# Kernel tuning notes

Hardware: AMD Instinct MI355X
Metric: run time of the kernel (lower is better)

Reference implementation:

```python
import jax, jax.numpy as jnp
import numpy as np

N, L, D = 2, 2048, 96
H, DK, DV = 4, 16, 16
OUT = 96
SPATIAL = H * (3 + 1 + 3)  # points + distance + direction per head
INF = 100000.0
EPS_DIR = 1e-10
EPS_LN = 1e-5


def setup_inputs() -> dict:
    key = jax.random.key(0)
    ks = jax.random.split(key, 10)
    return {
        "x": jax.random.normal(ks[0], (N, L, D), jnp.float32),
        "pos_CA": jax.random.normal(ks[1], (N, L, 3), jnp.float32),
        "pos_CB": jax.random.normal(ks[2], (N, L, 3), jnp.float32),
        "frame": jax.random.normal(ks[3], (N, L, 3, 3), jnp.float32),
        "mask": jnp.ones((N, L), dtype=bool),
        "Wq": jax.random.normal(ks[4], (D, H * DK), jnp.float32) * 0.1,
        "Wk": jax.random.normal(ks[5], (D, H * DK), jnp.float32) * 0.1,
        "Wv": jax.random.normal(ks[6], (D, H * DV), jnp.float32) * 0.1,
        "Wo": jax.random.normal(ks[7], (H * DV + SPATIAL, OUT), jnp.float32) * 0.1,
        "bo": jnp.zeros((OUT,), jnp.float32),
        "gamma": jnp.ones((OUT,), jnp.float32),
        "beta": jnp.zeros((OUT,), jnp.float32),
    }


def reference(x, pos_CA, pos_CB, frame, mask, Wq, Wk, Wv, Wo, bo, gamma, beta):
    n, l, _ = x.shape
    q = (x @ Wq).reshape(n, l, H, DK)
    k = (x @ Wk).reshape(n, l, H, DK)
    v = (x @ Wv).reshape(n, l, H, DV)

    # logits (N, L_q, L_k, H)
    logits = jnp.einsum('blhd,bkhd->blkh', q, k)
    mask_row = mask[:, :, None, None]           # (N, L, 1, 1)
    mask_pair = mask_row & mask[:, None, :, None]
    logits = jnp.where(mask_pair, logits, logits - INF)
    alpha = jax.nn.softmax(logits, axis=2)
    alpha = jnp.where(mask_row, alpha, 0.0)

    feat_node = jnp.einsum('blkh,bkhd->blhd', alpha, v).reshape(n, l, H * DV)

    # rel_pos[b,l,k] = CB[k] - CA[l]
    rel_pos = pos_CB[:, None, :, :] - pos_CA[:, :, None, :]
    atom_pos_bias = jnp.einsum('blkh,blkd->blhd', alpha, rel_pos)  # (N,L,H,3)
    feat_distance = jnp.linalg.norm(atom_pos_bias, axis=-1, keepdims=True)
    feat_points = jnp.einsum('blij,blhj->blhi', frame, atom_pos_bias)
    feat_direction = feat_points / (jnp.linalg.norm(feat_points, axis=-1, keepdims=True) + EPS_DIR)

    feat_spatial = jnp.concatenate([
        feat_points.reshape(n, l, H * 3),
        feat_distance.reshape(n, l, H),
        feat_direction.reshape(n, l, H * 3),
    ], axis=-1)

    feat_all = jnp.concatenate([feat_node, feat_spatial], axis=-1) @ Wo + bo
    feat_all = jnp.where(mask[:, :, None], feat_all, 0.0)

    # output_dim == input_dim -> residual + LayerNorm
    h = x + feat_all
    mu = jnp.mean(h, axis=-1, keepdims=True)
    var = jnp.var(h, axis=-1, keepdims=True)
    return (h - mu) / jnp.sqrt(var + EPS_LN) * gamma + beta
```

## Files before the change

kernel.cpp:

```cpp
#include <hip/hip_runtime.h>
#include <hip/hip_fp16.h>

typedef _Float16 f16;
typedef _Float16 v4h __attribute__((ext_vector_type(4)));
typedef short    v4s __attribute__((ext_vector_type(4)));
typedef short    v8s __attribute__((ext_vector_type(8)));
typedef float    v4f __attribute__((ext_vector_type(4)));

#define NB   2
#define LSEQ 2048
#define DIM  96
#define NH   4
#define ROWS 4096
#define NT16 128
#define NT32 64
#define OUTD 96
#define SHIFT 12.0f

#if __has_builtin(__builtin_amdgcn_mfma_f32_16x16x16f16)
#define MFMA16_F16(A, B, C) __builtin_amdgcn_mfma_f32_16x16x16f16((A), (B), (C), 0, 0, 0)
#else
static __device__ __forceinline__ v4f mfma16_f16_asm(v4h a, v4h b, v4f c) {
    asm volatile("v_mfma_f32_16x16x16_f16 %0, %1, %2, %0"
                 : "+v"(c) : "v"(a), "v"(b));
    return c;
}
#define MFMA16_F16(A, B, C) mfma16_f16_asm((A), (B), (C))
#endif
#define MFMA_BF16(A, B, C) __builtin_amdgcn_mfma_f32_16x16x32_bf16((A), (B), (C), 0, 0, 0)

static __device__ __forceinline__ short f2bf(float f) {
    unsigned u = __builtin_bit_cast(unsigned, f);
    u += 0x7FFF + ((u >> 16) & 1);
    return (short)(u >> 16);
}

__global__ __launch_bounds__(256) void proj_kernel(
    const float* __restrict__ x,
    const float* __restrict__ posCB,
    const float* __restrict__ Wq,
    const float* __restrict__ Wk,
    const float* __restrict__ Wv,
    f16*   __restrict__ qf,
    f16*   __restrict__ kf,
    short* __restrict__ vf,
    short* __restrict__ pf)
{
    const int w    = threadIdx.x >> 6;
    const int lane = threadIdx.x & 63;
    const int rowbase = blockIdx.x * 4;

    __shared__ float xs[4][DIM];
    __shared__ float part[4][4][64][3];

    xs[w][lane] = x[(size_t)(rowbase + w) * DIM + lane];
    if (lane < DIM - 64) xs[w][64 + lane] = x[(size_t)(rowbase + w) * DIM + 64 + lane];
    __syncthreads();

    float qa[4] = {0.f, 0.f, 0.f, 0.f};
    float ka[4] = {0.f, 0.f, 0.f, 0.f};
    float va[4] = {0.f, 0.f, 0.f, 0.f};
    const int d0 = w * 24;
    #pragma unroll 6
    for (int t = 0; t < 24; ++t) {
        const int dd = d0 + t;
        const float wqv = Wq[dd * 64 + lane];
        const float wkv = Wk[dd * 64 + lane];
        const float wvv = Wv[dd * 64 + lane];
        #pragma unroll
        for (int r = 0; r < 4; ++r) {
            const float xv = xs[r][dd];
            qa[r] = fmaf(xv, wqv, qa[r]);
            ka[r] = fmaf(xv, wkv, ka[r]);
            va[r] = fmaf(xv, wvv, va[r]);
        }
    }
    #pragma unroll
    for (int r = 0; r < 4; ++r) {
        part[w][r][lane][0] = qa[r];
        part[w][r][lane][1] = ka[r];
        part[w][r][lane][2] = va[r];
    }
    __syncthreads();

    float q = 0.f, k = 0.f, v = 0.f;
    #pragma unroll
    for (int w2 = 0; w2 < 4; ++w2) {
        q += part[w2][w][lane][0];
        k += part[w2][w][lane][1];
        v += part[w2][w][lane][2];
    }
    const int row = rowbase + w;
    const int b   = row >> 11;
    const int seq = row & (LSEQ - 1);
    const int h   = lane >> 4, d = lane & 15;
    const int bh  = b * NH + h;

    const int t16 = seq >> 4, m = seq & 15;
    const int idx16 = (m + 16 * (d >> 2)) * 4 + (d & 3);
    qf[((size_t)(bh * NT16 + t16)) * 256 + idx16] = (f16)q;
    kf[((size_t)(bh * NT16 + t16)) * 256 + idx16] = (f16)k;

    const int t32 = seq >> 5, kl = seq & 31;
    const int quadS = (kl & 15) >> 2;
    const int jS    = (kl < 16) ? (kl & 3) : 4 + (kl & 3);
    vf[((size_t)(bh * NT32 + t32)) * 512 + (d + 16 * quadS) * 8 + jS] = f2bf(v);

    if (blockIdx.x < NB * NT32) {
        const int b2 = blockIdx.x >> 6, t2 = blockIdx.x & 63;
        const int tid = threadIdx.x;
        const int lf = tid & 63, jh = tid >> 6;
        const int n = lf & 15, qS = lf >> 4;
        #pragma unroll
        for (int u = 0; u < 2; ++u) {
            const int jSp = jh * 2 + u;
            const int key = t2 * 32 + (jSp < 4 ? qS * 4 + jSp : 16 + qS * 4 + (jSp & 3));
            float val = 0.f;
            if (n < 3)       val = posCB[((size_t)(b2 * LSEQ + key)) * 3 + n];
            else if (n == 3) val = 1.f;
            pf[((size_t)(b2 * NT32 + t2)) * 512 + lf * 8 + jSp] = f2bf(val);
        }
    }
}

__global__ __launch_bounds__(1024, 1) void attn_epi_kernel(
    const f16*   __restrict__ qf,
    const f16*   __restrict__ kf,
    const short* __restrict__ vf,
    const short* __restrict__ pf,
    const float* __restrict__ x,
    const float* __restrict__ posCA,
    const float* __restrict__ frame,
    const float* __restrict__ Wo,
    const float* __restrict__ bo,
    const float* __restrict__ gamma,
    const float* __restrict__ beta,
    float*       __restrict__ out)
{
    const int w     = threadIdx.x >> 6;
    const int lane  = threadIdx.x & 63;
    const int head  = w & 3, kq = w >> 2;
    const int b     = blockIdx.x >> 7;
    const int qt    = blockIdx.x & 127;
    const int bh    = b * NH + head;
    const int quad  = lane >> 4, c16 = lane & 15;

    __shared__ float comb[16][64][12];
    __shared__ float feat[16][100];
    __shared__ float aps[16][NH][3];

    const v4h aq = *(const v4h*)(qf + ((size_t)(bh * NT16 + qt)) * 256 + lane * 4);
    const f16*   kb = kf + (size_t)bh * NT16 * 256;
    const short* vb = vf + (size_t)bh * NT32 * 512;
    const short* pb = pf + (size_t)b  * NT32 * 512;

    v4f O  = {0.f, 0.f, 0.f, 0.f};
    v4f Wa = {0.f, 0.f, 0.f, 0.f};
    const v4f zero = {0.f, 0.f, 0.f, 0.f};
    float psum = 0.f;

    #pragma unroll 2
    for (int i = 0; i < 16; ++i) {
        const int t32 = kq * 16 + i;
        const v4h bk0 = *(const v4h*)(kb + (size_t)(2 * t32    ) * 256 + lane * 4);
        const v4h bk1 = *(const v4h*)(kb + (size_t)(2 * t32 + 1) * 256 + lane * 4);
        const v8s bv  = *(const v8s*)(vb + (size_t)t32 * 512 + lane * 8);
        const v8s bp  = *(const v8s*)(pb + (size_t)t32 * 512 + lane * 8);

        const v4f S0 = MFMA16_F16(bk0, aq, zero);
        const v4f S1 = MFMA16_F16(bk1, aq, zero);

        v8s ap;
        #pragma unroll
        for (int r = 0; r < 4; ++r) {
            const float e0 = __expf(S0[r] - SHIFT);
            const float e1 = __expf(S1[r] - SHIFT);
            ap[r]     = f2bf(e0);
            ap[4 + r] = f2bf(e1);
            psum += e0 + e1;
        }
        O  = MFMA_BF16(ap, bv, O);
        Wa = MFMA_BF16(ap, bp, Wa);
    }

    {
        float* cb = &comb[w][lane][0];
        *(v4f*)cb       = O;
        *(v4f*)(cb + 4) = Wa;
        cb[8] = psum;
    }
    __syncthreads();

    const int rowg0 = b * LSEQ + qt * 16;

    if (w < 4) {
        #pragma unroll
        for (int k2 = 1; k2 < 4; ++k2) {
            const float* cb = &comb[k2 * 4 + w][lane][0];
            O    += *(const v4f*)cb;
            Wa   += *(const v4f*)(cb + 4);
            psum += cb[8];
        }
        psum += __shfl_xor(psum, 16);
        psum += __shfl_xor(psum, 32);
        const float inv = 1.f / psum;
        #pragma unroll
        for (int r = 0; r < 4; ++r) {
            const float ir = __shfl(inv, quad * 4 + r);
            feat[quad * 4 + r][w * 16 + c16] = O[r] * ir;
            if (c16 < 3)
                aps[quad * 4 + r][w][c16] = Wa[r] * ir;
        }
    }
    __syncthreads();

    if (lane < 4) {
        const int hh = lane;
        const int grow = rowg0 + w;
        float apb[3];
        #pragma unroll
        for (int j = 0; j < 3; ++j)
            apb[j] = aps[w][hh][j] - posCA[(size_t)grow * 3 + j];
        const float dist = sqrtf(apb[0]*apb[0] + apb[1]*apb[1] + apb[2]*apb[2]);
        float fp[3];
        #pragma unroll
        for (int i = 0; i < 3; ++i) {
            float a = 0.f;
            #pragma unroll
            for (int j = 0; j < 3; ++j)
                a = fmaf(frame[(size_t)grow * 9 + i * 3 + j], apb[j], a);
            fp[i] = a;
        }
        const float fpn  = sqrtf(fp[0]*fp[0] + fp[1]*fp[1] + fp[2]*fp[2]);
        const float rinv = 1.f / (fpn + 1e-10f);
        #pragma unroll
        for (int i = 0; i < 3; ++i) {
            feat[w][64 + hh * 3 + i] = fp[i];
            feat[w][80 + hh * 3 + i] = fp[i] * rinv;
        }
        feat[w][76 + hh] = dist;
    }
    __syncthreads();

    {
        const int grow = rowg0 + w;

        float acc0 = bo[lane];
        #pragma unroll 8
        for (int r2 = 0; r2 < 92; ++r2)
            acc0 = fmaf(feat[w][r2], Wo[r2 * OUTD + lane], acc0);
        const float hv0 = acc0 + x[(size_t)grow * DIM + lane];

        float hv1 = 0.f;
        if (lane < 32) {
            float acc1 = bo[64 + lane];
            #pragma unroll 8
            for (int r2 = 0; r2 < 92; ++r2)
                acc1 = fmaf(feat[w][r2], Wo[r2 * OUTD + 64 + lane], acc1);
            hv1 = acc1 + x[(size_t)grow * DIM + 64 + lane];
        }

        float ls = hv0 + hv1;
        float lq = fmaf(hv0, hv0, hv1 * hv1);
        #pragma unroll
        for (int off = 32; off > 0; off >>= 1) {
            ls += __shfl_xor(ls, off);
            lq += __shfl_xor(lq, off);
        }
        const float mu  = ls * (1.f / OUTD);
        const float var = lq * (1.f / OUTD) - mu * mu;
        const float rs  = rsqrtf(var + 1e-5f);

        out[(size_t)grow * OUTD + lane] = (hv0 - mu) * rs * gamma[lane] + beta[lane];
        if (lane < 32)
            out[(size_t)grow * OUTD + 64 + lane] =
                (hv1 - mu) * rs * gamma[64 + lane] + beta[64 + lane];
    }
}

extern "C" void kernel_launch(void* const* d_in, const int* in_sizes, int n_in,
                              void* d_out, int out_size, void* d_ws, size_t ws_size,
                              hipStream_t stream)
{
    const float* x     = (const float*)d_in[0];
    const float* posCA = (const float*)d_in[1];
    const float* posCB = (const float*)d_in[2];
    const float* frame = (const float*)d_in[3];
    const float* Wq    = (const float*)d_in[5];
    const float* Wk    = (const float*)d_in[6];
    const float* Wv    = (const float*)d_in[7];
    const float* Wo    = (const float*)d_in[8];
    const float* bo    = (const float*)d_in[9];
    const float* gamma = (const float*)d_in[10];
    const float* beta  = (const float*)d_in[11];

    f16*   qf = (f16*)d_ws;
    f16*   kf = qf + (size_t)8 * NT16 * 256;
    short* vf = (short*)(kf + (size_t)8 * NT16 * 256);
    short* pf = vf + (size_t)8 * NT32 * 512;

    proj_kernel<<<ROWS / 4, 256, 0, stream>>>(x, posCB, Wq, Wk, Wv, qf, kf, vf, pf);
    attn_epi_kernel<<<NB * NT16, 1024, 0, stream>>>(qf, kf, vf, pf,
                                                    x, posCA, frame,
                                                    Wo, bo, gamma, beta,
                                                    (float*)d_out);
}
```

Before: 105.3 us.

## Use MFMA for QKV projection, pack K tiles pairwise, prefetch attention loads

The QKV projection now runs on f16 MFMA, with 16 rows per block and weights staged into LDS fragments. It replaces the scalar FMA loop and its cross-wave LDS reduction, and launches 256 blocks instead of 1024. K is stored in a packed 32-key layout so one 8-wide load feeds both score MFMAs. The attention loop software-prefetches the next tile's K/V/P and uses exp2 with a folded log2e and shift. Every block re-converts the full weight matrices into LDS, and rounding x and W to f16 slightly changes precision.

```diff
diff --git a/kernel.cpp b/kernel.cpp
--- a/kernel.cpp
+++ b/kernel.cpp
@@ -3,6 +3,7 @@
 
 typedef _Float16 f16;
 typedef _Float16 v4h __attribute__((ext_vector_type(4)));
+typedef _Float16 v8h __attribute__((ext_vector_type(8)));
 typedef short    v4s __attribute__((ext_vector_type(4)));
 typedef short    v8s __attribute__((ext_vector_type(8)));
 typedef float    v4f __attribute__((ext_vector_type(4)));
@@ -16,6 +17,8 @@
 #define NT32 64
 #define OUTD 96
 #define SHIFT 12.0f
+#define LOG2E   1.4426950408889634f
+#define NSH2    (-17.312340490667562f)
 
 #if __has_builtin(__builtin_amdgcn_mfma_f32_16x16x16f16)
 #define MFMA16_F16(A, B, C) __builtin_amdgcn_mfma_f32_16x16x16f16((A), (B), (C), 0, 0, 0)
@@ -27,7 +30,14 @@
 }
 #define MFMA16_F16(A, B, C) mfma16_f16_asm((A), (B), (C))
 #endif
-#define MFMA_BF16(A, B, C) __builtin_amdgcn_mfma_f32_16x16x32_bf16((A), (B), (C), 0, 0, 0)
+#define MFMA32_F16(A, B, C) __builtin_amdgcn_mfma_f32_16x16x32_f16((A), (B), (C), 0, 0, 0)
+#define MFMA_BF16(A, B, C)  __builtin_amdgcn_mfma_f32_16x16x32_bf16((A), (B), (C), 0, 0, 0)
+
+#if __has_builtin(__builtin_amdgcn_exp2f)
+#define EXP2F(x) __builtin_amdgcn_exp2f(x)
+#else
+#define EXP2F(x) exp2f(x)
+#endif
 
 static __device__ __forceinline__ short f2bf(float f) {
     unsigned u = __builtin_bit_cast(unsigned, f);
@@ -42,78 +52,87 @@
     const float* __restrict__ Wk,
     const float* __restrict__ Wv,
     f16*   __restrict__ qf,
-    f16*   __restrict__ kf,
+    f16*   __restrict__ kf2,
     short* __restrict__ vf,
     short* __restrict__ pf)
 {
-    const int w    = threadIdx.x >> 6;
-    const int lane = threadIdx.x & 63;
-    const int rowbase = blockIdx.x * 4;
-
-    __shared__ float xs[4][DIM];
-    __shared__ float part[4][4][64][3];
-
-    xs[w][lane] = x[(size_t)(rowbase + w) * DIM + lane];
-    if (lane < DIM - 64) xs[w][64 + lane] = x[(size_t)(rowbase + w) * DIM + 64 + lane];
+    const int tid  = threadIdx.x;
+    const int wv   = tid >> 6;
+    const int lane = tid & 63;
+    const int quad = lane >> 4, c16 = lane & 15;
+    const int bid  = blockIdx.x;
+    const int b    = bid >> 7, t16 = bid & 127;
+    const int row0 = bid * 16;
+
+    __shared__ v8h wfragv[12 * 3 * 65];
+    f16* wf = (f16*)wfragv;
+
+    v8h xb[3];
+    #pragma unroll
+    for (int kt = 0; kt < 3; ++kt) {
+        const float* xp = x + (size_t)(row0 + c16) * DIM + kt * 32 + quad * 8;
+        const v4f x0 = *(const v4f*)xp;
+        const v4f x1 = *(const v4f*)(xp + 4);
+        v8h h;
+        #pragma unroll
+        for (int j = 0; j < 4; ++j) { h[j] = (f16)x0[j]; h[4 + j] = (f16)x1[j]; }
+        xb[kt] = h;
+    }
+
+    {
+        const float* Ws[3] = {Wq, Wk, Wv};
+        #pragma unroll
+        for (int widx = 0; widx < 3; ++widx) {
+            const float* W = Ws[widx];
+            #pragma unroll
+            for (int it = 0; it < 24; ++it) {
+                const int flat = it * 256 + tid;
+                const int dd = flat >> 6, n = flat & 63;
+                const int frag = (widx * 4 + (n >> 4)) * 3 + (dd >> 5);
+                wf[frag * 520 + (((dd >> 3) & 3) * 16 + (n & 15)) * 8 + (dd & 7)]
+                    = (f16)W[flat];
+            }
+        }
+    }
     __syncthreads();
 
-    float qa[4] = {0.f, 0.f, 0.f, 0.f};
-    float ka[4] = {0.f, 0.f, 0.f, 0.f};
-    float va[4] = {0.f, 0.f, 0.f, 0.f};
-    const int d0 = w * 24;
-    #pragma unroll 6
-    for (int t = 0; t < 24; ++t) {
-        const int dd = d0 + t;
-        const float wqv = Wq[dd * 64 + lane];
-        const float wkv = Wk[dd * 64 + lane];
-        const float wvv = Wv[dd * 64 + lane];
-        #pragma unroll
-        for (int r = 0; r < 4; ++r) {
-            const float xv = xs[r][dd];
-            qa[r] = fmaf(xv, wqv, qa[r]);
-            ka[r] = fmaf(xv, wkv, ka[r]);
-            va[r] = fmaf(xv, wvv, va[r]);
-        }
-    }
     #pragma unroll
-    for (int r = 0; r < 4; ++r) {
-        part[w][r][lane][0] = qa[r];
-        part[w][r][lane][1] = ka[r];
-        part[w][r][lane][2] = va[r];
-    }
-    __syncthreads();
-
-    float q = 0.f, k = 0.f, v = 0.f;
-    #pragma unroll
-    for (int w2 = 0; w2 < 4; ++w2) {
-        q += part[w2][w][lane][0];
-        k += part[w2][w][lane][1];
-        v += part[w2][w][lane][2];
-    }
-    const int row = rowbase + w;
-    const int b   = row >> 11;
-    const int seq = row & (LSEQ - 1);
-    const int h   = lane >> 4, d = lane & 15;
-    const int bh  = b * NH + h;
-
-    const int t16 = seq >> 4, m = seq & 15;
-    const int idx16 = (m + 16 * (d >> 2)) * 4 + (d & 3);
-    qf[((size_t)(bh * NT16 + t16)) * 256 + idx16] = (f16)q;
-    kf[((size_t)(bh * NT16 + t16)) * 256 + idx16] = (f16)k;
-
-    const int t32 = seq >> 5, kl = seq & 31;
-    const int quadS = (kl & 15) >> 2;
-    const int jS    = (kl < 16) ? (kl & 3) : 4 + (kl & 3);
-    vf[((size_t)(bh * NT32 + t32)) * 512 + (d + 16 * quadS) * 8 + jS] = f2bf(v);
-
-    if (blockIdx.x < NB * NT32) {
-        const int b2 = blockIdx.x >> 6, t2 = blockIdx.x & 63;
-        const int tid = threadIdx.x;
+    for (int u = 0; u < 3; ++u) {
+        const int dt = wv * 3 + u;
+        v4f acc = {0.f, 0.f, 0.f, 0.f};
+        #pragma unroll
+        for (int kt = 0; kt < 3; ++kt)
+            acc = MFMA32_F16(wfragv[(dt * 3 + kt) * 65 + lane], xb[kt], acc);
+
+        const int widx = dt >> 2, sub = dt & 3;
+        const int bh = b * NH + sub;
+        if (widx == 0) {
+            v4h o;
+            #pragma unroll
+            for (int r = 0; r < 4; ++r) o[r] = (f16)acc[r];
+            *(v4h*)(qf + ((size_t)(bh * NT16 + t16)) * 256 + (c16 + 16 * quad) * 4) = o;
+        } else if (widx == 1) {
+            v4h o;
+            #pragma unroll
+            for (int r = 0; r < 4; ++r) o[r] = (f16)acc[r];
+            *(v4h*)(kf2 + ((size_t)(bh * NT32 + (t16 >> 1))) * 512
+                        + lane * 8 + (t16 & 1) * 4) = o;
+        } else {
+            short* dst = vf + ((size_t)(bh * NT32 + (t16 >> 1))) * 512
+                            + (t16 & 1) * 4 + (c16 & 3);
+            #pragma unroll
+            for (int r = 0; r < 4; ++r)
+                dst[(quad * 4 + r + 16 * (c16 >> 2)) * 8] = f2bf(acc[r]);
+        }
+    }
+
+    if (bid < NB * NT32) {
+        const int b2 = bid >> 6, t2 = bid & 63;
         const int lf = tid & 63, jh = tid >> 6;
         const int n = lf & 15, qS = lf >> 4;
         #pragma unroll
-        for (int u = 0; u < 2; ++u) {
-            const int jSp = jh * 2 + u;
+        for (int u2 = 0; u2 < 2; ++u2) {
+            const int jSp = jh * 2 + u2;
             const int key = t2 * 32 + (jSp < 4 ? qS * 4 + jSp : 16 + qS * 4 + (jSp & 3));
             float val = 0.f;
             if (n < 3)       val = posCB[((size_t)(b2 * LSEQ + key)) * 3 + n];
@@ -125,7 +144,7 @@
 
 __global__ __launch_bounds__(1024, 1) void attn_epi_kernel(
     const f16*   __restrict__ qf,
-    const f16*   __restrict__ kf,
+    const f16*   __restrict__ kf2,
     const short* __restrict__ vf,
     const short* __restrict__ pf,
     const float* __restrict__ x,
@@ -150,38 +169,49 @@
     __shared__ float aps[16][NH][3];
 
     const v4h aq = *(const v4h*)(qf + ((size_t)(bh * NT16 + qt)) * 256 + lane * 4);
-    const f16*   kb = kf + (size_t)bh * NT16 * 256;
-    const short* vb = vf + (size_t)bh * NT32 * 512;
-    const short* pb = pf + (size_t)b  * NT32 * 512;
+    const f16*   kb = kf2 + (size_t)bh * NT32 * 512;
+    const short* vb = vf  + (size_t)bh * NT32 * 512;
+    const short* pb = pf  + (size_t)b  * NT32 * 512;
 
     v4f O  = {0.f, 0.f, 0.f, 0.f};
     v4f Wa = {0.f, 0.f, 0.f, 0.f};
     const v4f zero = {0.f, 0.f, 0.f, 0.f};
     float psum = 0.f;
 
-    #pragma unroll 2
-    for (int i = 0; i < 16; ++i) {
-        const int t32 = kq * 16 + i;
-        const v4h bk0 = *(const v4h*)(kb + (size_t)(2 * t32    ) * 256 + lane * 4);
-        const v4h bk1 = *(const v4h*)(kb + (size_t)(2 * t32 + 1) * 256 + lane * 4);
-        const v8s bv  = *(const v8s*)(vb + (size_t)t32 * 512 + lane * 8);
-        const v8s bp  = *(const v8s*)(pb + (size_t)t32 * 512 + lane * 8);
-
-        const v4f S0 = MFMA16_F16(bk0, aq, zero);
-        const v4f S1 = MFMA16_F16(bk1, aq, zero);
-
-        v8s ap;
-        #pragma unroll
-        for (int r = 0; r < 4; ++r) {
-            const float e0 = __expf(S0[r] - SHIFT);
-            const float e1 = __expf(S1[r] - SHIFT);
-            ap[r]     = f2bf(e0);
-            ap[4 + r] = f2bf(e1);
-            psum += e0 + e1;
-        }
-        O  = MFMA_BF16(ap, bv, O);
-        Wa = MFMA_BF16(ap, bp, Wa);
-    }
+    const int t0 = kq * 16;
+    v8h bk = *(const v8h*)(kb + (size_t)t0 * 512 + lane * 8);
+    v8s bv = *(const v8s*)(vb + (size_t)t0 * 512 + lane * 8);
+    v8s bp = *(const v8s*)(pb + (size_t)t0 * 512 + lane * 8);
+
+#define ATTN_STEP(BK, BV, BP) do {                                          \
+        const v4h bk0 = __builtin_shufflevector((BK), (BK), 0, 1, 2, 3);    \
+        const v4h bk1 = __builtin_shufflevector((BK), (BK), 4, 5, 6, 7);    \
+        const v4f S0 = MFMA16_F16(bk0, aq, zero);                           \
+        const v4f S1 = MFMA16_F16(bk1, aq, zero);                           \
+        v8s ap;                                                             \
+        _Pragma("unroll")                                                   \
+        for (int r = 0; r < 4; ++r) {                                       \
+            const float e0 = EXP2F(fmaf(S0[r], LOG2E, NSH2));               \
+            const float e1 = EXP2F(fmaf(S1[r], LOG2E, NSH2));               \
+            ap[r]     = f2bf(e0);                                           \
+            ap[4 + r] = f2bf(e1);                                           \
+            psum += e0 + e1;                                                \
+        }                                                                   \
+        O  = MFMA_BF16(ap, (BV), O);                                        \
+        Wa = MFMA_BF16(ap, (BP), Wa);                                       \
+    } while (0)
+
+    #pragma unroll 3
+    for (int i = 0; i < 15; ++i) {
+        const v8h bkc = bk; const v8s bvc = bv, bpc = bp;
+        const size_t off = (size_t)(t0 + i + 1) * 512 + lane * 8;
+        bk = *(const v8h*)(kb + off);
+        bv = *(const v8s*)(vb + off);
+        bp = *(const v8s*)(pb + off);
+        ATTN_STEP(bkc, bvc, bpc);
+    }
+    ATTN_STEP(bk, bv, bp);
+#undef ATTN_STEP
 
     {
         float* cb = &comb[w][lane][0];
@@ -294,13 +324,13 @@
     const float* gamma = (const float*)d_in[10];
     const float* beta  = (const float*)d_in[11];
 
-    f16*   qf = (f16*)d_ws;
-    f16*   kf = qf + (size_t)8 * NT16 * 256;
-    short* vf = (short*)(kf + (size_t)8 * NT16 * 256);
-    short* pf = vf + (size_t)8 * NT32 * 512;
-
-    proj_kernel<<<ROWS / 4, 256, 0, stream>>>(x, posCB, Wq, Wk, Wv, qf, kf, vf, pf);
-    attn_epi_kernel<<<NB * NT16, 1024, 0, stream>>>(qf, kf, vf, pf,
+    f16*   qf  = (f16*)d_ws;
+    f16*   kf2 = qf + (size_t)8 * NT16 * 256;
+    short* vf  = (short*)(kf2 + (size_t)8 * NT32 * 512);
+    short* pf  = vf + (size_t)8 * NT32 * 512;
+
+    proj_kernel<<<256, 256, 0, stream>>>(x, posCB, Wq, Wk, Wv, qf, kf2, vf, pf);
+    attn_epi_kernel<<<NB * NT16, 1024, 0, stream>>>(qf, kf2, vf, pf,
                                                     x, posCA, frame,
                                                     Wo, bo, gamma, beta,
                                                     (float*)d_out);
```

Measured after the change: 104.8 us. About the same (-0.5%).
